# Performance work log

Hardware: AMD Instinct MI355X
Metric: run time of the kernel (lower is better)

Reference implementation:

```python
import jax, jax.numpy as jnp
import numpy as np

BILATERAL = True
THETA_ALPHA = 8.0   # spatial bandwidth for bilateral term
THETA_BETA = 0.5    # color bandwidth for bilateral term
THETA_GAMMA = 3.0   # spatial bandwidth for spatial-only term


def _features(input_image):
    # input_image: [B, Ci, H, W] -> features [B, N, D]
    B, Ci, H, W = input_image.shape
    N = H * W
    ys, xs = jnp.meshgrid(jnp.arange(H, dtype=jnp.float32),
                          jnp.arange(W, dtype=jnp.float32), indexing='ij')
    pos = jnp.stack([ys, xs], axis=-1).reshape(N, 2)  # [N, 2]
    if BILATERAL:
        sp = jnp.broadcast_to(pos / THETA_ALPHA, (B, N, 2))
        col = input_image.reshape(B, Ci, N).transpose(0, 2, 1) / THETA_BETA  # [B, N, Ci]
        return jnp.concatenate([sp, col], axis=-1)  # [B, N, 2+Ci]
    else:
        return jnp.broadcast_to(pos / THETA_GAMMA, (B, N, 2))


def _gauss_filter(values, feats):
    # values: [B, C, N]; feats: [B, N, D] -> [B, C, N]
    # K_ij = exp(-0.5 * ||f_i - f_j||^2) (unnormalized, as in permutohedral filtering)
    sq = jnp.sum(feats * feats, axis=-1)  # [B, N]
    # squared distances: [B, N, N]
    d2 = sq[:, :, None] + sq[:, None, :] - 2.0 * jnp.einsum('bnd,bmd->bnm', feats, feats)
    K = jnp.exp(-0.5 * jnp.maximum(d2, 0.0))
    return jnp.einsum('bnm,bcm->bcn', K, values)


def setup_inputs() -> dict:
    key = jax.random.key(0)
    k1, k2 = jax.random.split(key)
    cur_state = jax.random.normal(k1, (2, 21, 96, 96), dtype=jnp.float32)
    input_image = jax.random.uniform(k2, (2, 3, 96, 96), dtype=jnp.float32)
    return {"cur_state": cur_state, "input_image": input_image}


def reference(cur_state, input_image):
    assert cur_state.ndim == 4
    B, C, H, W = cur_state.shape
    N = H * W
    feats = _features(input_image)                 # [B, N, D]
    vals = cur_state.reshape(B, C, N)              # [B, C, N]
    out = _gauss_filter(vals, feats)               # [B, C, N]
    return out.reshape(B, C, H, W)
```

## Files before the change

kernel.cpp:

```cpp
#include <hip/hip_runtime.h>
#include <hip/hip_bf16.h>
#include <math.h>


#define HH 96
#define WW 96
#define NN (HH * WW)
#define NB 2
#define NC 21

typedef __attribute__((ext_vector_type(8))) short short8;
typedef __attribute__((ext_vector_type(16))) float f32x16;

constexpr float INV_TA = 0.125f;
constexpr float INV_TB = 2.0f;
constexpr float LOG2E  = 1.44269504088896340736f;

constexpr int BLK   = 256;
constexpr int ITILE = 128;
constexpr int NIT   = NN / ITILE;
constexpr int NJB   = NN / 32;
constexpr int G     = 24;
constexpr int QW    = NJB / G;

constexpr size_t VG_BYTES = (size_t)NB * NJB * 128 * 16;
constexpr size_t FJA_OFF  = VG_BYTES;

constexpr int NVU = NB * NJB * 128;
constexpr int NFT = NB * NN;
constexpr int NZ  = NB * NC * NN / 4;
constexpr int PREP_TASKS = NVU + NFT + NZ;

#if defined(__has_builtin)
#if __has_builtin(__builtin_amdgcn_exp2f)
#define EXP2F(x) __builtin_amdgcn_exp2f(x)
#endif
#endif
#ifndef EXP2F
#define EXP2F(x) exp2f(x)
#endif

__device__ __forceinline__ unsigned short bf16_rne(float f) {
    __hip_bfloat16 h = __float2bfloat16(f);
    unsigned short u; __builtin_memcpy(&u, &h, 2); return u;
}
__device__ __forceinline__ float bf16_f(unsigned short u) {
    __hip_bfloat16 h; __builtin_memcpy(&h, &u, 2); return __bfloat162float(h);
}
__device__ __forceinline__ unsigned pk2(float a, float b) {
    const unsigned u0 = __float_as_uint(a) + 0x8000u;
    const unsigned u1 = __float_as_uint(b) + 0x8000u;
    return __builtin_amdgcn_perm(u1, u0, 0x07060302u);
}
__device__ __forceinline__ unsigned pkrn(float a, float b) {
    __hip_bfloat162 h = __float22bfloat162_rn(float2{a, b});
    unsigned u; __builtin_memcpy(&u, &h, 4); return u;
}

__global__ __launch_bounds__(BLK)
void prep_kernel(const float* __restrict__ cur, const float* __restrict__ img,
                 unsigned char* __restrict__ ws, float* __restrict__ out) {
    const int t = blockIdx.x * BLK + threadIdx.x;
    if (t < NVU) {
        const int c    = t & 31;
        const int h    = (t >> 5) & 1;
        const int m    = (t >> 6) & 1;
        const int jw   = t >> 7;
        const int b    = jw / NJB;
        const int jblk = jw % NJB;
        const int jb = jblk * 32 + m * 16 + 4 * h;
        float4 qa = {0, 0, 0, 0}, qb = {0, 0, 0, 0};
        if (c < NC) {
            const float* row = cur + ((size_t)b * NC + c) * NN;
            qa = *(const float4*)(row + jb);
            qb = *(const float4*)(row + jb + 8);
        }
        uint4 o;
        o.x = pk2(qa.x, qa.y); o.y = pk2(qa.z, qa.w);
        o.z = pk2(qb.x, qb.y); o.w = pk2(qb.z, qb.w);
        *(uint4*)(ws + (size_t)t * 16) = o;
    } else if (t < NVU + NFT) {
        const int tf = t - NVU;
        const int b = tf / NN;
        const int j = tf % NN;
        const float y = (float)(j / WW) * INV_TA;
        const float x = (float)(j % WW) * INV_TA;
        const float* ib = img + (size_t)b * 3 * NN;
        unsigned short ch[3], cl[3]; float cf[3];
        #pragma unroll
        for (int d = 0; d < 3; ++d) {
            const float c = ib[d * NN + j] * INV_TB;
            ch[d] = bf16_rne(c);
            const float chf = bf16_f(ch[d]);
            cl[d] = bf16_rne(c - chf);
            cf[d] = chf + bf16_f(cl[d]);
        }
        const float e = -0.5f * (y * y + x * x +
                                 cf[0] * cf[0] + cf[1] * cf[1] + cf[2] * cf[2]);
        const unsigned short eh = bf16_rne(e);
        const unsigned short el = bf16_rne(e - bf16_f(eh));
        const unsigned short yb = bf16_rne(y), xb = bf16_rne(x);
        const unsigned short one = 0x3F80;
        unsigned short* u0 = (unsigned short*)
            (ws + FJA_OFF + ((size_t)(b * 2 + 0) * NN + j) * 16);
        unsigned short* u1 = (unsigned short*)
            (ws + FJA_OFF + ((size_t)(b * 2 + 1) * NN + j) * 16);
        u0[0] = yb; u0[1] = xb; u0[2] = ch[0]; u0[3] = ch[1]; u0[4] = ch[2];
        u0[5] = cl[0]; u0[6] = cl[1]; u0[7] = cl[2];
        u1[0] = ch[0]; u1[1] = ch[1]; u1[2] = ch[2]; u1[3] = eh; u1[4] = el;
        u1[5] = one; u1[6] = one; u1[7] = 0;
    } else {
        ((float4*)out)[t - NVU - NFT] = float4{0.0f, 0.0f, 0.0f, 0.0f};
    }
}

__global__ __launch_bounds__(BLK, 2)
void perm_gauss_mfma(const float* __restrict__ img,
                     const unsigned char* __restrict__ ws,
                     float* __restrict__ out) {
    __shared__ __align__(16) float tile[4 * 32 * 33];
    const int tid  = threadIdx.x;
    const int lane = tid & 63;
    const int wave = tid >> 6;
    const int il   = lane & 31;
    const int half = lane >> 5;

    const int it = blockIdx.x, g = blockIdx.y, b = blockIdx.z;
    const int ibase = it * ITILE + wave * 32;
    const float* imgb = img + (size_t)b * 3 * NN;
    float* outb = out + (size_t)b * NC * NN;

    const int ig = ibase + il;
    const float y = (float)(ig / WW) * INV_TA;
    const float x = (float)(ig % WW) * INV_TA;
    unsigned short ch[3], cl[3]; float cf[3];
    #pragma unroll
    for (int d = 0; d < 3; ++d) {
        const float c = imgb[d * NN + ig] * INV_TB;
        ch[d] = bf16_rne(c);
        const float chf = bf16_f(ch[d]);
        cl[d] = bf16_rne(c - chf);
        cf[d] = chf + bf16_f(cl[d]);
    }
    const float e = -0.5f * (y * y + x * x +
                             cf[0] * cf[0] + cf[1] * cf[1] + cf[2] * cf[2]);
    const unsigned short eh = bf16_rne(e);
    const unsigned short el = bf16_rne(e - bf16_f(eh));
    const unsigned short one = 0x3F80;
    union { unsigned short u[8]; short8 v; } bfi;
    if (half == 0) {
        bfi.u[0] = bf16_rne(y); bfi.u[1] = bf16_rne(x);
        bfi.u[2] = ch[0]; bfi.u[3] = ch[1]; bfi.u[4] = ch[2];
        bfi.u[5] = ch[0]; bfi.u[6] = ch[1]; bfi.u[7] = ch[2];
    } else {
        bfi.u[0] = cl[0]; bfi.u[1] = cl[1]; bfi.u[2] = cl[2];
        bfi.u[3] = one; bfi.u[4] = one; bfi.u[5] = eh; bfi.u[6] = el;
        bfi.u[7] = 0;
    }

    f32x16 acc, zz;
    #pragma unroll
    for (int r = 0; r < 16; ++r) { acc[r] = 0.0f; zz[r] = 0.0f; }

    const int jb0 = g * QW;
    const unsigned char* fp = ws + FJA_OFF +
        ((size_t)(b * 2 + half) * NN + (size_t)jb0 * 32 + il) * 16;
    const unsigned char* vp = ws +
        ((size_t)(b * NJB + jb0) * 128 + half * 32 + il) * 16;

    auto consume = [&](const f32x16& s, short8 V1, short8 V2) {
        float w[16];
        #pragma unroll
        for (int r = 0; r < 16; ++r) w[r] = EXP2F(s[r] * LOG2E);
        union { unsigned dw[4]; short8 v; } a1, a2;
        #pragma unroll
        for (int d = 0; d < 4; ++d) {
            a1.dw[d] = pkrn(w[2 * d],     w[2 * d + 1]);
            a2.dw[d] = pkrn(w[8 + 2 * d], w[9 + 2 * d]);
        }
        acc = __builtin_amdgcn_mfma_f32_32x32x16_bf16(a1.v, V1, acc, 0, 0, 0);
        acc = __builtin_amdgcn_mfma_f32_32x32x16_bf16(a2.v, V2, acc, 0, 0, 0);
    };

    short8 af0 = *(const short8*)fp;
    short8 af1 = *(const short8*)(fp + 512);
    short8 v1  = *(const short8*)vp;
    short8 v2  = *(const short8*)(vp + 1024);
    f32x16 s_cur = __builtin_amdgcn_mfma_f32_32x32x16_bf16(af0, bfi.v, zz, 0, 0, 0);

    #pragma unroll 2
    for (int q = 0; q < QW - 1; ++q) {
        const f32x16 s_next =
            __builtin_amdgcn_mfma_f32_32x32x16_bf16(af1, bfi.v, zz, 0, 0, 0);
        if (q < QW - 2) af1 = *(const short8*)(fp + 1024);
        fp += 512;
        const short8 v1n = *(const short8*)(vp + 2048);
        const short8 v2n = *(const short8*)(vp + 2048 + 1024);
        vp += 2048;
        consume(s_cur, v1, v2);
        s_cur = s_next; v1 = v1n; v2 = v2n;
    }
    consume(s_cur, v1, v2);

    float* mytile = tile + wave * (32 * 33);
    #pragma unroll
    for (int r = 0; r < 16; ++r) {
        const int row = (r & 3) + 8 * (r >> 2) + 4 * half;
        mytile[row * 33 + il] = acc[r];
    }
    #pragma unroll
    for (int cc = 0; cc < 11; ++cc) {
        const int c = 2 * cc + half;
        if (c < NC) {
            const float v = mytile[il * 33 + c];
            atomicAdd(&outb[(size_t)c * NN + ibase + il], v);
        }
    }
}

extern "C" void kernel_launch(void* const* d_in, const int* in_sizes, int n_in,
                              void* d_out, int out_size, void* d_ws, size_t ws_size,
                              hipStream_t stream) {
    const float* cur = (const float*)d_in[0];
    const float* img = (const float*)d_in[1];
    float* out = (float*)d_out;
    unsigned char* ws = (unsigned char*)d_ws;

    prep_kernel<<<PREP_TASKS / BLK, BLK, 0, stream>>>(cur, img, ws, out);
    dim3 grid(NIT, G, NB);
    perm_gauss_mfma<<<grid, BLK, 0, stream>>>(img, ws, out);
}
```

Baseline: 94.55 us.

## Process two i-tiles per wave to reuse loaded j-features and values

Each wave now handles 64 output pixels (two 32-row i-tiles) instead of 32. Every j-block's feature and value fragments are loaded once and reused for both tiles, halving global loads per unit of work and halving the grid's x dimension. The cost is doubled accumulator and score register pressure, which may reduce occupancy under the 2-blocks-per-CU launch bound. The shared-memory transpose and atomic epilogue now run twice per wave, the second pass reusing the same tile buffer for the second accumulator.

Result: slower. 98.94 us (+4.6%).

```diff
diff --git a/kernel.cpp b/kernel.cpp
--- a/kernel.cpp
+++ b/kernel.cpp
@@ -17,7 +17,7 @@
 constexpr float LOG2E  = 1.44269504088896340736f;
 
 constexpr int BLK   = 256;
-constexpr int ITILE = 128;
+constexpr int ITILE = 256;
 constexpr int NIT   = NN / ITILE;
 constexpr int NJB   = NN / 32;
 constexpr int G     = 24;
@@ -126,41 +126,45 @@
     const int half = lane >> 5;
 
     const int it = blockIdx.x, g = blockIdx.y, b = blockIdx.z;
-    const int ibase = it * ITILE + wave * 32;
+    const int ibase = it * ITILE + wave * 64;
     const float* imgb = img + (size_t)b * 3 * NN;
     float* outb = out + (size_t)b * NC * NN;
 
-    const int ig = ibase + il;
-    const float y = (float)(ig / WW) * INV_TA;
-    const float x = (float)(ig % WW) * INV_TA;
-    unsigned short ch[3], cl[3]; float cf[3];
-    #pragma unroll
-    for (int d = 0; d < 3; ++d) {
-        const float c = imgb[d * NN + ig] * INV_TB;
-        ch[d] = bf16_rne(c);
-        const float chf = bf16_f(ch[d]);
-        cl[d] = bf16_rne(c - chf);
-        cf[d] = chf + bf16_f(cl[d]);
-    }
-    const float e = -0.5f * (y * y + x * x +
-                             cf[0] * cf[0] + cf[1] * cf[1] + cf[2] * cf[2]);
-    const unsigned short eh = bf16_rne(e);
-    const unsigned short el = bf16_rne(e - bf16_f(eh));
-    const unsigned short one = 0x3F80;
-    union { unsigned short u[8]; short8 v; } bfi;
-    if (half == 0) {
-        bfi.u[0] = bf16_rne(y); bfi.u[1] = bf16_rne(x);
-        bfi.u[2] = ch[0]; bfi.u[3] = ch[1]; bfi.u[4] = ch[2];
-        bfi.u[5] = ch[0]; bfi.u[6] = ch[1]; bfi.u[7] = ch[2];
-    } else {
-        bfi.u[0] = cl[0]; bfi.u[1] = cl[1]; bfi.u[2] = cl[2];
-        bfi.u[3] = one; bfi.u[4] = one; bfi.u[5] = eh; bfi.u[6] = el;
-        bfi.u[7] = 0;
-    }
-
-    f32x16 acc, zz;
-    #pragma unroll
-    for (int r = 0; r < 16; ++r) { acc[r] = 0.0f; zz[r] = 0.0f; }
+    auto make_bfi = [&](int ig) {
+        const float y = (float)(ig / WW) * INV_TA;
+        const float x = (float)(ig % WW) * INV_TA;
+        unsigned short ch[3], cl[3]; float cf[3];
+        #pragma unroll
+        for (int d = 0; d < 3; ++d) {
+            const float c = imgb[d * NN + ig] * INV_TB;
+            ch[d] = bf16_rne(c);
+            const float chf = bf16_f(ch[d]);
+            cl[d] = bf16_rne(c - chf);
+            cf[d] = chf + bf16_f(cl[d]);
+        }
+        const float e = -0.5f * (y * y + x * x +
+                                 cf[0] * cf[0] + cf[1] * cf[1] + cf[2] * cf[2]);
+        const unsigned short eh = bf16_rne(e);
+        const unsigned short el = bf16_rne(e - bf16_f(eh));
+        const unsigned short one = 0x3F80;
+        union { unsigned short u[8]; short8 v; } r;
+        if (half == 0) {
+            r.u[0] = bf16_rne(y); r.u[1] = bf16_rne(x);
+            r.u[2] = ch[0]; r.u[3] = ch[1]; r.u[4] = ch[2];
+            r.u[5] = ch[0]; r.u[6] = ch[1]; r.u[7] = ch[2];
+        } else {
+            r.u[0] = cl[0]; r.u[1] = cl[1]; r.u[2] = cl[2];
+            r.u[3] = one; r.u[4] = one; r.u[5] = eh; r.u[6] = el;
+            r.u[7] = 0;
+        }
+        return r.v;
+    };
+    const short8 bfiA = make_bfi(ibase + il);
+    const short8 bfiB = make_bfi(ibase + 32 + il);
+
+    f32x16 accA, accB, zz;
+    #pragma unroll
+    for (int r = 0; r < 16; ++r) { accA[r] = 0.0f; accB[r] = 0.0f; zz[r] = 0.0f; }
 
     const int jb0 = g * QW;
     const unsigned char* fp = ws + FJA_OFF +
@@ -168,7 +172,7 @@
     const unsigned char* vp = ws +
         ((size_t)(b * NJB + jb0) * 128 + half * 32 + il) * 16;
 
-    auto consume = [&](const f32x16& s, short8 V1, short8 V2) {
+    auto consume = [&](const f32x16& s, short8 V1, short8 V2, f32x16& acc) {
         float w[16];
         #pragma unroll
         for (int r = 0; r < 16; ++r) w[r] = EXP2F(s[r] * LOG2E);
@@ -182,31 +186,38 @@
         acc = __builtin_amdgcn_mfma_f32_32x32x16_bf16(a2.v, V2, acc, 0, 0, 0);
     };
 
-    short8 af0 = *(const short8*)fp;
-    short8 af1 = *(const short8*)(fp + 512);
-    short8 v1  = *(const short8*)vp;
-    short8 v2  = *(const short8*)(vp + 1024);
-    f32x16 s_cur = __builtin_amdgcn_mfma_f32_32x32x16_bf16(af0, bfi.v, zz, 0, 0, 0);
+    short8 af_cur = *(const short8*)fp;
+    short8 af_nxt = *(const short8*)(fp + 512);
+    short8 v1 = *(const short8*)vp;
+    short8 v2 = *(const short8*)(vp + 1024);
+    f32x16 sA_cur = __builtin_amdgcn_mfma_f32_32x32x16_bf16(af_cur, bfiA, zz, 0, 0, 0);
 
     #pragma unroll 2
     for (int q = 0; q < QW - 1; ++q) {
-        const f32x16 s_next =
-            __builtin_amdgcn_mfma_f32_32x32x16_bf16(af1, bfi.v, zz, 0, 0, 0);
-        if (q < QW - 2) af1 = *(const short8*)(fp + 1024);
+        const f32x16 sB = __builtin_amdgcn_mfma_f32_32x32x16_bf16(af_cur, bfiB, zz, 0, 0, 0);
+        const f32x16 sA_nxt = __builtin_amdgcn_mfma_f32_32x32x16_bf16(af_nxt, bfiA, zz, 0, 0, 0);
+        short8 af_nn = af_nxt;
+        if (q < QW - 2) af_nn = *(const short8*)(fp + 1024);
         fp += 512;
         const short8 v1n = *(const short8*)(vp + 2048);
         const short8 v2n = *(const short8*)(vp + 2048 + 1024);
         vp += 2048;
-        consume(s_cur, v1, v2);
-        s_cur = s_next; v1 = v1n; v2 = v2n;
-    }
-    consume(s_cur, v1, v2);
+        consume(sA_cur, v1, v2, accA);
+        consume(sB,     v1, v2, accB);
+        sA_cur = sA_nxt; af_cur = af_nxt; af_nxt = af_nn;
+        v1 = v1n; v2 = v2n;
+    }
+    {
+        const f32x16 sB = __builtin_amdgcn_mfma_f32_32x32x16_bf16(af_cur, bfiB, zz, 0, 0, 0);
+        consume(sA_cur, v1, v2, accA);
+        consume(sB,     v1, v2, accB);
+    }
 
     float* mytile = tile + wave * (32 * 33);
     #pragma unroll
     for (int r = 0; r < 16; ++r) {
         const int row = (r & 3) + 8 * (r >> 2) + 4 * half;
-        mytile[row * 33 + il] = acc[r];
+        mytile[row * 33 + il] = accA[r];
     }
     #pragma unroll
     for (int cc = 0; cc < 11; ++cc) {
@@ -214,6 +225,19 @@
         if (c < NC) {
             const float v = mytile[il * 33 + c];
             atomicAdd(&outb[(size_t)c * NN + ibase + il], v);
+        }
+    }
+    #pragma unroll
+    for (int r = 0; r < 16; ++r) {
+        const int row = (r & 3) + 8 * (r >> 2) + 4 * half;
+        mytile[row * 33 + il] = accB[r];
+    }
+    #pragma unroll
+    for (int cc = 0; cc < 11; ++cc) {
+        const int c = 2 * cc + half;
+        if (c < NC) {
+            const float v = mytile[il * 33 + c];
+            atomicAdd(&outb[(size_t)c * NN + ibase + 32 + il], v);
         }
     }
 }
```
